# Kernel tuning notes

Hardware: AMD Instinct MI355X
Metric: run time of the kernel (lower is better)

## Reference

```python
import jax, jax.numpy as jnp
import numpy as np

N_NODES = 50000
N_EDGES = 600000
D_IN = 128
D_HID = 128
N_IDX = 4096


def gcn_conv(x, W, b, edge_index, num_nodes):
    """PyG GCNConv: add self loops, symmetric deg normalization, scatter-add, bias."""
    h = x @ W  # [N, D_out]
    loop = jnp.arange(num_nodes, dtype=edge_index.dtype)
    src = jnp.concatenate([edge_index[0], loop])
    dst = jnp.concatenate([edge_index[1], loop])
    deg = jax.ops.segment_sum(jnp.ones_like(dst, dtype=h.dtype), dst, num_segments=num_nodes)
    dinv = jnp.where(deg > 0, jax.lax.rsqrt(jnp.maximum(deg, 1.0)), 0.0)
    norm = dinv[src] * dinv[dst]  # [E+N]
    msgs = h[src] * norm[:, None]
    out = jax.ops.segment_sum(msgs, dst, num_segments=num_nodes)
    return out + b


def setup_inputs() -> dict:
    key = jax.random.key(0)
    ks = jax.random.split(key, 18)
    d = {
        "x": jax.random.normal(ks[0], (N_NODES, D_IN), dtype=jnp.float32),
        "syntactic_edge_index": jax.random.randint(ks[1], (2, N_EDGES), 0, N_NODES, dtype=jnp.int32),
        "sequential_edge_index": jax.random.randint(ks[2], (2, N_EDGES), 0, N_NODES, dtype=jnp.int32),
        "semantic_edge_index": jax.random.randint(ks[3], (2, N_EDGES), 0, N_NODES, dtype=jnp.int32),
        "index": jax.random.randint(ks[4], (N_IDX,), 0, N_NODES, dtype=jnp.int32),
    }
    s = 1.0 / np.sqrt(D_IN)
    names = ["syn", "seq", "sem"]
    for i, n in enumerate(names):
        d[f"w1_{n}"] = jax.random.uniform(ks[5 + i], (D_IN, D_HID), jnp.float32, -s, s)
        d[f"b1_{n}"] = jnp.zeros((D_HID,), jnp.float32)
        d[f"w2_{n}"] = jax.random.uniform(ks[8 + i], (D_HID, D_HID), jnp.float32, -s, s)
        d[f"b2_{n}"] = jnp.zeros((D_HID,), jnp.float32)
    return d


def reference(x, syntactic_edge_index, sequential_edge_index, semantic_edge_index, index,
              w1_syn, b1_syn, w1_seq, b1_seq, w1_sem, b1_sem,
              w2_syn, b2_syn, w2_seq, b2_seq, w2_sem, b2_sem):
    n = x.shape[0]
    # layer 1: three parallel GCN branches + ReLU (dropout is identity in eval mode)
    a = jax.nn.relu(gcn_conv(x, w1_syn, b1_syn, syntactic_edge_index, n))
    b = jax.nn.relu(gcn_conv(x, w1_seq, b1_seq, sequential_edge_index, n))
    c = jax.nn.relu(gcn_conv(x, w1_sem, b1_sem, semantic_edge_index, n))
    h = jnp.maximum(jnp.maximum(a, b), c)
    # layer 2
    a2 = jax.nn.relu(gcn_conv(h, w2_syn, b2_syn, syntactic_edge_index, n))
    b2 = jax.nn.relu(gcn_conv(h, w2_seq, b2_seq, sequential_edge_index, n))
    c2 = jax.nn.relu(gcn_conv(h, w2_sem, b2_sem, semantic_edge_index, n))
    out = jnp.maximum(jnp.maximum(a2, b2), c2)
    return out[index]
```

## Files before the change

### kernel.cpp

```cpp
#include <hip/hip_runtime.h>
#include <hip/hip_fp16.h>

#define NN 50000
#define NE 600000
#define NG 3
#define D  128
#define NI 4096
#define BW 1024
#define NBUCK 49
#define EPT_BIN 16
#define EPB_BIN (256 * EPT_BIN)
#define NBLK_BIN ((NE + EPB_BIN - 1) / EPB_BIN)

typedef _Float16 half8 __attribute__((ext_vector_type(8)));
typedef _Float16 half4v __attribute__((ext_vector_type(4)));
typedef float floatx4 __attribute__((ext_vector_type(4)));

static __device__ __forceinline__ float wextract(unsigned int v) {
  unsigned short u = (unsigned short)(v >> 16);
  _Float16 h;
  __builtin_memcpy(&h, &u, 2);
  return (float)h;
}

static __device__ __forceinline__ unsigned int packsw(int s, float w) {
  _Float16 h = (_Float16)w;
  unsigned short u;
  __builtin_memcpy(&u, &h, 2);
  return (unsigned int)s | ((unsigned int)u << 16);
}


__global__ __launch_bounds__(256) void xcvt_kernel(const float* __restrict__ x,
    __half* __restrict__ xh, int n2) {
  int i = blockIdx.x * 256 + threadIdx.x;
  if (i >= n2) return;
  float2 v = ((const float2*)x)[i];
  ((__half2*)xh)[i] = __floats2half2_rn(v.x, v.y);
}

__global__ __launch_bounds__(256) void wcvt_kernel(
    const float* __restrict__ W0, const float* __restrict__ W1, const float* __restrict__ W2,
    const float* __restrict__ W3, const float* __restrict__ W4, const float* __restrict__ W5,
    __half* __restrict__ Wf) {
  const float* Wm[6] = {W0, W1, W2, W3, W4, W5};
  int t = blockIdx.x * 256 + threadIdx.x;
  if (t >= 6 * 2048) return;
  int mat = t >> 11;
  int fr = (t >> 6) & 31;
  int lane = t & 63;
  int tt = fr >> 2, ks = fr & 3;
  int n = tt * 16 + (lane & 15);
  int kb = ks * 32 + (lane >> 4) * 8;
  const float* W = Wm[mat];
#pragma unroll
  for (int j = 0; j < 8; j++)
    Wf[(size_t)t * 8 + j] = __float2half(W[(kb + j) * 128 + n]);
}


__global__ __launch_bounds__(256) void count_kernel(const int* __restrict__ e0,
    const int* __restrict__ e1, const int* __restrict__ e2, int* __restrict__ bucketCnt) {
  __shared__ int cnt[NBUCK];
  int g = blockIdx.y;
  const int* ei = (g == 0) ? e0 : ((g == 1) ? e1 : e2);
  int tid = threadIdx.x;
  if (tid < NBUCK) cnt[tid] = 0;
  __syncthreads();
  int base = blockIdx.x * EPB_BIN;
#pragma unroll
  for (int i = 0; i < EPT_BIN; i++) {
    int e = base + tid + i * 256;
    if (e < NE) atomicAdd(&cnt[ei[NE + e] >> 10], 1);
  }
  __syncthreads();
  if (tid < NBUCK) atomicAdd(&bucketCnt[g * NBUCK + tid], cnt[tid]);
}

__global__ void bscan_kernel(const int* __restrict__ bucketCnt, int* __restrict__ bucketBase,
                             int* __restrict__ cursor, int* __restrict__ rp) {
  int g = threadIdx.x;
  if (g >= NG) return;
  int run = 0;
  for (int b = 0; b < NBUCK; b++) {
    int c = bucketCnt[g * NBUCK + b];
    bucketBase[g * NBUCK + b] = run;
    cursor[g * NBUCK + b] = run;
    run += c;
  }
  rp[g * (NN + 1) + NN] = NE;
}

__global__ __launch_bounds__(256) void bin_kernel(const int* __restrict__ e0,
    const int* __restrict__ e1, const int* __restrict__ e2,
    int* __restrict__ cursor, unsigned int* __restrict__ binned) {
  __shared__ int cnt[NBUCK];
  __shared__ int base[NBUCK];
  int g = blockIdx.y;
  const int* ei = (g == 0) ? e0 : ((g == 1) ? e1 : e2);
  int tid = threadIdx.x;
  if (tid < NBUCK) cnt[tid] = 0;
  __syncthreads();
  int estart = blockIdx.x * EPB_BIN;
  int src[EPT_BIN], dst[EPT_BIN], rk[EPT_BIN];
#pragma unroll
  for (int i = 0; i < EPT_BIN; i++) {
    int e = estart + tid + i * 256;
    if (e < NE) {
      src[i] = ei[e];
      dst[i] = ei[NE + e];
      rk[i] = atomicAdd(&cnt[dst[i] >> 10], 1);
    } else {
      rk[i] = -1;
    }
  }
  __syncthreads();
  if (tid < NBUCK) base[tid] = (cnt[tid] > 0) ? atomicAdd(&cursor[g * NBUCK + tid], cnt[tid]) : 0;
  __syncthreads();
#pragma unroll
  for (int i = 0; i < EPT_BIN; i++) {
    if (rk[i] >= 0) {
      int b = dst[i] >> 10;
      binned[(size_t)g * NE + base[b] + rk[i]] =
          (unsigned int)src[i] | ((unsigned int)dst[i] << 16);
    }
  }
}

__global__ __launch_bounds__(256) void csr_kernel(const unsigned int* __restrict__ binned,
    const int* __restrict__ bucketBase, const int* __restrict__ bucketCnt,
    int* __restrict__ rp, float* __restrict__ dinv) {
  __shared__ int deg[BW];
  __shared__ int wsum[4];
  int g = blockIdx.y, b = blockIdx.x;
  int tid = threadIdx.x;
  int node0 = b * BW;
  int bb = bucketBase[g * NBUCK + b];
  int total = bucketCnt[g * NBUCK + b];
  const unsigned int* bp = binned + (size_t)g * NE + bb;
  for (int i = tid; i < BW; i += 256) deg[i] = 0;
  __syncthreads();
  for (int e = tid; e < total; e += 256) {
    unsigned int p = bp[e];
    atomicAdd(&deg[(int)(p >> 16) - node0], 1);
  }
  __syncthreads();
  int d0 = deg[tid * 4], d1 = deg[tid * 4 + 1], d2 = deg[tid * 4 + 2], d3 = deg[tid * 4 + 3];
  int s = d0 + d1 + d2 + d3;
  int lane = tid & 63;
  int incl = s;
#pragma unroll
  for (int off = 1; off < 64; off <<= 1) {
    int n = __shfl_up(incl, off, 64);
    if (lane >= off) incl += n;
  }
  if (lane == 63) wsum[tid >> 6] = incl;
  __syncthreads();
  int wbase = 0;
#pragma unroll
  for (int w = 0; w < 4; w++)
    if (w < (tid >> 6)) wbase += wsum[w];
  int ex = wbase + incl - s;
  int exs[4] = {ex, ex + d0, ex + d0 + d1, ex + d0 + d1 + d2};
  int ds[4] = {d0, d1, d2, d3};
#pragma unroll
  for (int k = 0; k < 4; k++) {
    int node = node0 + tid * 4 + k;
    if (node < NN) {
      rp[g * (NN + 1) + node] = bb + exs[k];
      dinv[g * NN + node] = rsqrtf((float)ds[k] + 1.0f);
    }
  }
}

__global__ __launch_bounds__(256) void fillp_kernel(const unsigned int* __restrict__ binned,
    const int* __restrict__ bucketBase, const int* __restrict__ bucketCnt,
    const int* __restrict__ rp, const float* __restrict__ dinv,
    unsigned int* __restrict__ colp) {
  __shared__ int cur[BW];
  int g = blockIdx.y, b = blockIdx.x;
  int tid = threadIdx.x;
  int node0 = b * BW;
  int bb = bucketBase[g * NBUCK + b];
  int total = bucketCnt[g * NBUCK + b];
  const unsigned int* bp = binned + (size_t)g * NE + bb;
  for (int i = tid; i < BW; i += 256) {
    int node = node0 + i;
    cur[i] = (node < NN) ? rp[g * (NN + 1) + node] : 0;
  }
  __syncthreads();
  for (int e = tid; e < total; e += 256) {
    unsigned int p = bp[e];
    int srcid = (int)(p & 0xffffu);
    int r = atomicAdd(&cur[(int)(p >> 16) - node0], 1);
    colp[(size_t)g * NE + r] = packsw(srcid, dinv[g * NN + srcid]);
  }
}


__global__ __launch_bounds__(256) void aggf_kernel(
    const __half* __restrict__ srch, const int* __restrict__ rp,
    const unsigned int* __restrict__ colp, const float* __restrict__ dinv,
    const int* __restrict__ index, __half* __restrict__ tout, int nrows) {
  int w = (blockIdx.x * 256 + threadIdx.x) >> 6;
  if (w >= nrows) return;
  int lane = threadIdx.x & 63;
  int sub = lane >> 5;
  int fl = lane & 31;
  int node = index ? index[w] : w;
  const _Float16* srcv = (const _Float16*)srch;
  half4v selfh = *(const half4v*)&srcv[(size_t)node * D + fl * 4];
  float di0 = dinv[node], di1 = dinv[NN + node], di2 = dinv[2 * NN + node];
  float a0[4], a1[4], a2[4];
#pragma unroll
  for (int k = 0; k < 4; k++) {
    float sv = sub ? 0.f : (float)selfh[k];
    a0[k] = di0 * sv; a1[k] = di1 * sv; a2[k] = di2 * sv;
  }
  int s0 = rp[node],                e0 = rp[node + 1];
  int s1 = rp[(NN + 1) + node],     e1 = rp[(NN + 1) + node + 1];
  int s2 = rp[2 * (NN + 1) + node], e2 = rp[2 * (NN + 1) + node + 1];
  int n0 = e0 - s0, n1 = e1 - s1, n2 = e2 - s2;
  unsigned int c0 = (lane < n0) ? colp[s0 + lane] : 0u;
  unsigned int c1 = (lane < n1) ? colp[NE + s1 + lane] : 0u;
  unsigned int c2 = (lane < n2) ? colp[2 * NE + s2 + lane] : 0u;
  int m0 = min(n0, 64), m1 = min(n1, 64), m2 = min(n2, 64);
  int mx = max(m0, max(m1, m2));
  for (int j = 0; j < mx; j += 8) {
    half4v h0[4], h1[4], h2[4];
    float w0[4], w1[4], w2[4];
    bool p0 = j < m0, p1 = j < m1, p2 = j < m2;
    if (p0) {
#pragma unroll
      for (int u = 0; u < 4; u++) {
        unsigned int v = (unsigned int)__shfl((int)c0, j + u * 2 + sub, 64);
        w0[u] = wextract(v);
        h0[u] = *(const half4v*)&srcv[(size_t)(v & 0xffffu) * D + fl * 4];
      }
    }
    if (p1) {
#pragma unroll
      for (int u = 0; u < 4; u++) {
        unsigned int v = (unsigned int)__shfl((int)c1, j + u * 2 + sub, 64);
        w1[u] = wextract(v);
        h1[u] = *(const half4v*)&srcv[(size_t)(v & 0xffffu) * D + fl * 4];
      }
    }
    if (p2) {
#pragma unroll
      for (int u = 0; u < 4; u++) {
        unsigned int v = (unsigned int)__shfl((int)c2, j + u * 2 + sub, 64);
        w2[u] = wextract(v);
        h2[u] = *(const half4v*)&srcv[(size_t)(v & 0xffffu) * D + fl * 4];
      }
    }
    if (p0) {
#pragma unroll
      for (int u = 0; u < 4; u++)
#pragma unroll
        for (int k = 0; k < 4; k++) a0[k] = fmaf((float)h0[u][k], w0[u], a0[k]);
    }
    if (p1) {
#pragma unroll
      for (int u = 0; u < 4; u++)
#pragma unroll
        for (int k = 0; k < 4; k++) a1[k] = fmaf((float)h1[u][k], w1[u], a1[k]);
    }
    if (p2) {
#pragma unroll
      for (int u = 0; u < 4; u++)
#pragma unroll
        for (int k = 0; k < 4; k++) a2[k] = fmaf((float)h2[u][k], w2[u], a2[k]);
    }
  }
  for (int q = s0 + 64; q < e0; q += 64) {
    int nn = min(e0 - q, 64);
    unsigned int c = (lane < nn) ? colp[q + lane] : 0u;
    for (int j = 0; j < nn; j += 2) {
      unsigned int v = (unsigned int)__shfl((int)c, j + sub, 64);
      float wf = wextract(v);
      half4v hv = *(const half4v*)&srcv[(size_t)(v & 0xffffu) * D + fl * 4];
#pragma unroll
      for (int k = 0; k < 4; k++) a0[k] = fmaf((float)hv[k], wf, a0[k]);
    }
  }
  for (int q = s1 + 64; q < e1; q += 64) {
    int nn = min(e1 - q, 64);
    unsigned int c = (lane < nn) ? colp[NE + q + lane] : 0u;
    for (int j = 0; j < nn; j += 2) {
      unsigned int v = (unsigned int)__shfl((int)c, j + sub, 64);
      float wf = wextract(v);
      half4v hv = *(const half4v*)&srcv[(size_t)(v & 0xffffu) * D + fl * 4];
#pragma unroll
      for (int k = 0; k < 4; k++) a1[k] = fmaf((float)hv[k], wf, a1[k]);
    }
  }
  for (int q = s2 + 64; q < e2; q += 64) {
    int nn = min(e2 - q, 64);
    unsigned int c = (lane < nn) ? colp[2 * NE + q + lane] : 0u;
    for (int j = 0; j < nn; j += 2) {
      unsigned int v = (unsigned int)__shfl((int)c, j + sub, 64);
      float wf = wextract(v);
      half4v hv = *(const half4v*)&srcv[(size_t)(v & 0xffffu) * D + fl * 4];
#pragma unroll
      for (int k = 0; k < 4; k++) a2[k] = fmaf((float)hv[k], wf, a2[k]);
    }
  }
#pragma unroll
  for (int k = 0; k < 4; k++) {
    a0[k] += __shfl_xor(a0[k], 32, 64);
    a1[k] += __shfl_xor(a1[k], 32, 64);
    a2[k] += __shfl_xor(a2[k], 32, 64);
  }
  if (sub == 0) {
    size_t stride = (size_t)nrows * D;
    _Float16* tv = (_Float16*)tout;
    half4v o0, o1, o2;
#pragma unroll
    for (int k = 0; k < 4; k++) {
      o0[k] = (_Float16)(di0 * a0[k]);
      o1[k] = (_Float16)(di1 * a1[k]);
      o2[k] = (_Float16)(di2 * a2[k]);
    }
    *(half4v*)&tv[(size_t)w * D + fl * 4]              = o0;
    *(half4v*)&tv[stride + (size_t)w * D + fl * 4]     = o1;
    *(half4v*)&tv[2 * stride + (size_t)w * D + fl * 4] = o2;
  }
}


__global__ __launch_bounds__(256) void mmf_kernel(const __half* __restrict__ A,
    const __half* __restrict__ Wf,
    const float* __restrict__ B0, const float* __restrict__ B1, const float* __restrict__ B2,
    __half* __restrict__ outh, float* __restrict__ outf, int M) {
  __shared__ _Float16 Ws[16384];
  const float* Bb[3] = {B0, B1, B2};
  const int tid = threadIdx.x;
  const int wave = tid >> 6, lane = tid & 63;
  const int wr = (wave >> 1) * 64, wc = (wave & 1) * 64;
  const int ln = lane & 15, quad = lane >> 4;
  const int row_base = blockIdx.x * 128 + wr;
  float om[4][4][4];

  for (int b = 0; b < 3; b++) {
    const __half* Wb = Wf + (size_t)b * 16384;
#pragma unroll
    for (int i = 0; i < 8; i++) {
      int id = tid + i * 256;
      *(half8*)&Ws[id * 8] = *(const half8*)&Wb[(size_t)id * 8];
    }
    __syncthreads();

    const __half* Ab = A + (size_t)b * M * D;
    float bias[4];
#pragma unroll
    for (int ct = 0; ct < 4; ct++) bias[ct] = Bb[b][wc + ct * 16 + ln];
    floatx4 acc[4][4];
#pragma unroll
    for (int rt = 0; rt < 4; rt++)
#pragma unroll
      for (int ct = 0; ct < 4; ct++)
        acc[rt][ct] = (floatx4){bias[ct], bias[ct], bias[ct], bias[ct]};

#pragma unroll
    for (int ks = 0; ks < 4; ks++) {
      half8 av[4];
#pragma unroll
      for (int rt = 0; rt < 4; rt++) {
        int r = row_base + rt * 16 + ln;
        r = (r < M) ? r : (M - 1);
        av[rt] = *(const half8*)&Ab[(size_t)r * D + ks * 32 + quad * 8];
      }
#pragma unroll
      for (int ct = 0; ct < 4; ct++) {
        int tt = (wc >> 4) + ct;
        half8 bv = *(const half8*)&Ws[((tt * 4 + ks) * 64 + lane) * 8];
#pragma unroll
        for (int rt = 0; rt < 4; rt++)
          acc[rt][ct] = __builtin_amdgcn_mfma_f32_16x16x32_f16(av[rt], bv, acc[rt][ct], 0, 0, 0);
      }
    }
#pragma unroll
    for (int rt = 0; rt < 4; rt++)
#pragma unroll
      for (int ct = 0; ct < 4; ct++)
#pragma unroll
        for (int r = 0; r < 4; r++) {
          float v = fmaxf(acc[rt][ct][r], 0.f);
          om[rt][ct][r] = (b == 0) ? v : fmaxf(om[rt][ct][r], v);
        }
    __syncthreads();
  }
#pragma unroll
  for (int rt = 0; rt < 4; rt++) {
    int m = row_base + rt * 16 + quad * 4;
#pragma unroll
    for (int r = 0; r < 4; r++) {
      if (m + r < M) {
#pragma unroll
        for (int ct = 0; ct < 4; ct++) {
          int n = wc + ct * 16 + ln;
          if (outh) outh[(size_t)(m + r) * D + n] = __float2half(om[rt][ct][r]);
          else      outf[(size_t)(m + r) * D + n] = om[rt][ct][r];
        }
      }
    }
  }
}


extern "C" void kernel_launch(void* const* d_in, const int* in_sizes, int n_in,
                              void* d_out, int out_size, void* d_ws, size_t ws_size,
                              hipStream_t stream) {
  const float* x = (const float*)d_in[0];
  const int* e0 = (const int*)d_in[1];
  const int* e1 = (const int*)d_in[2];
  const int* e2 = (const int*)d_in[3];
  const int* index = (const int*)d_in[4];
  const float* w1[3] = {(const float*)d_in[5], (const float*)d_in[9],  (const float*)d_in[13]};
  const float* b1[3] = {(const float*)d_in[6], (const float*)d_in[10], (const float*)d_in[14]};
  const float* w2[3] = {(const float*)d_in[7], (const float*)d_in[11], (const float*)d_in[15]};
  const float* b2[3] = {(const float*)d_in[8], (const float*)d_in[12], (const float*)d_in[16]};
  float* out = (float*)d_out;

  char* ws = (char*)d_ws;
  size_t o = 0;
  auto alloc = [&](size_t bytes) {
    o = (o + 255) & ~(size_t)255;
    void* p = ws + o;
    o += bytes;
    return p;
  };
  int*    rp     = (int*)alloc((size_t)NG * (NN + 1) * 4);
  unsigned int* colp = (unsigned int*)alloc((size_t)NG * NE * 4);
  float*  dinv   = (float*)alloc((size_t)NG * NN * 4);
  int*    bcnt   = (int*)alloc((size_t)NG * NBUCK * 4);
  int*    bbase  = (int*)alloc((size_t)NG * NBUCK * 4);
  int*    bcur   = (int*)alloc((size_t)NG * NBUCK * 4);
  __half* xh     = (__half*)alloc((size_t)NN * D * 2);
  __half* Wf     = (__half*)alloc((size_t)6 * 128 * 128 * 2);
  __half* t1     = (__half*)alloc((size_t)NG * NN * D * 2);
  __half* hacc   = (__half*)alloc((size_t)NN * D * 2);
  unsigned int* binned = (unsigned int*)t1;
  __half* t2     = t1;
  (void)ws_size; (void)in_sizes; (void)n_in; (void)out_size;

  hipMemsetAsync(bcnt, 0, (size_t)NG * NBUCK * 4, stream);
  xcvt_kernel<<<(NN * D / 2 + 255) / 256, 256, 0, stream>>>(x, xh, NN * D / 2);
  wcvt_kernel<<<48, 256, 0, stream>>>(w1[0], w1[1], w1[2], w2[0], w2[1], w2[2], Wf);
  count_kernel<<<dim3(NBLK_BIN, NG), 256, 0, stream>>>(e0, e1, e2, bcnt);
  bscan_kernel<<<1, 64, 0, stream>>>(bcnt, bbase, bcur, rp);
  bin_kernel<<<dim3(NBLK_BIN, NG), 256, 0, stream>>>(e0, e1, e2, bcur, binned);
  csr_kernel<<<dim3(NBUCK, NG), 256, 0, stream>>>(binned, bbase, bcnt, rp, dinv);
  fillp_kernel<<<dim3(NBUCK, NG), 256, 0, stream>>>(binned, bbase, bcnt, rp, dinv, colp);

  aggf_kernel<<<(NN * 64 + 255) / 256, 256, 0, stream>>>(xh, rp, colp, dinv, nullptr, t1, NN);
  mmf_kernel<<<(NN + 127) / 128, 256, 0, stream>>>(t1, Wf, b1[0], b1[1], b1[2],
                                                   hacc, nullptr, NN);
  aggf_kernel<<<(NI * 64 + 255) / 256, 256, 0, stream>>>(hacc, rp, colp, dinv, index, t2, NI);
  mmf_kernel<<<(NI + 127) / 128, 256, 0, stream>>>(t2, Wf + (size_t)3 * 16384,
                                                   b2[0], b2[1], b2[2], nullptr, out, NI);
}
```

Baseline: 297.5 us.

## Fuse prep kernels, widen aggregation gathers to half8, stage A tile in LDS

Merges the x conversion, weight conversion and edge bucket counting into one prep kernel with block-range dispatch, removing two launches and vectorizing the x conversion to 8 elements per thread. The aggregation kernel now has each lane gather 8 halves (16 bytes), so four edges are processed at once per wave instead of two. This needs an extra cross-quarter shuffle reduction and more accumulator registers. The mmf kernel stages the 128x128 A tile into padded shared memory before the MFMA loop instead of reading it from global per wave, raising LDS use to about 67 KB, which may reduce occupancy.

```diff
diff --git a/kernel.cpp b/kernel.cpp
--- a/kernel.cpp
+++ b/kernel.cpp
@@ -11,9 +11,11 @@
 #define EPT_BIN 16
 #define EPB_BIN (256 * EPT_BIN)
 #define NBLK_BIN ((NE + EPB_BIN - 1) / EPB_BIN)
+#define XCVT_BLKS 3125
+#define WCVT_BLKS 48
+#define CNT_BLKS (NBLK_BIN * NG)
 
 typedef _Float16 half8 __attribute__((ext_vector_type(8)));
-typedef _Float16 half4v __attribute__((ext_vector_type(4)));
 typedef float floatx4 __attribute__((ext_vector_type(4)));
 
 static __device__ __forceinline__ float wextract(unsigned int v) {
@@ -31,50 +33,53 @@
 }
 
 
-__global__ __launch_bounds__(256) void xcvt_kernel(const float* __restrict__ x,
-    __half* __restrict__ xh, int n2) {
-  int i = blockIdx.x * 256 + threadIdx.x;
-  if (i >= n2) return;
-  float2 v = ((const float2*)x)[i];
-  ((__half2*)xh)[i] = __floats2half2_rn(v.x, v.y);
-}
-
-__global__ __launch_bounds__(256) void wcvt_kernel(
+__global__ __launch_bounds__(256) void prep_kernel(
+    const float* __restrict__ x, __half* __restrict__ xh,
     const float* __restrict__ W0, const float* __restrict__ W1, const float* __restrict__ W2,
     const float* __restrict__ W3, const float* __restrict__ W4, const float* __restrict__ W5,
-    __half* __restrict__ Wf) {
-  const float* Wm[6] = {W0, W1, W2, W3, W4, W5};
-  int t = blockIdx.x * 256 + threadIdx.x;
-  if (t >= 6 * 2048) return;
-  int mat = t >> 11;
-  int fr = (t >> 6) & 31;
-  int lane = t & 63;
-  int tt = fr >> 2, ks = fr & 3;
-  int n = tt * 16 + (lane & 15);
-  int kb = ks * 32 + (lane >> 4) * 8;
-  const float* W = Wm[mat];
-#pragma unroll
-  for (int j = 0; j < 8; j++)
-    Wf[(size_t)t * 8 + j] = __float2half(W[(kb + j) * 128 + n]);
-}
-
-
-__global__ __launch_bounds__(256) void count_kernel(const int* __restrict__ e0,
-    const int* __restrict__ e1, const int* __restrict__ e2, int* __restrict__ bucketCnt) {
+    __half* __restrict__ Wf,
+    const int* __restrict__ e0, const int* __restrict__ e1, const int* __restrict__ e2,
+    int* __restrict__ bucketCnt) {
   __shared__ int cnt[NBUCK];
-  int g = blockIdx.y;
-  const int* ei = (g == 0) ? e0 : ((g == 1) ? e1 : e2);
+  int blk = blockIdx.x;
   int tid = threadIdx.x;
-  if (tid < NBUCK) cnt[tid] = 0;
-  __syncthreads();
-  int base = blockIdx.x * EPB_BIN;
-#pragma unroll
-  for (int i = 0; i < EPT_BIN; i++) {
-    int e = base + tid + i * 256;
-    if (e < NE) atomicAdd(&cnt[ei[NE + e] >> 10], 1);
-  }
-  __syncthreads();
-  if (tid < NBUCK) atomicAdd(&bucketCnt[g * NBUCK + tid], cnt[tid]);
+  if (blk < XCVT_BLKS) {
+    int i = blk * 256 + tid;
+    size_t base = (size_t)i * 8;
+    float4 v0 = *(const float4*)&x[base];
+    float4 v1 = *(const float4*)&x[base + 4];
+    half8 h;
+    h[0] = (_Float16)v0.x; h[1] = (_Float16)v0.y; h[2] = (_Float16)v0.z; h[3] = (_Float16)v0.w;
+    h[4] = (_Float16)v1.x; h[5] = (_Float16)v1.y; h[6] = (_Float16)v1.z; h[7] = (_Float16)v1.w;
+    *(half8*)&xh[base] = h;
+  } else if (blk < XCVT_BLKS + WCVT_BLKS) {
+    const float* Wm[6] = {W0, W1, W2, W3, W4, W5};
+    int t = (blk - XCVT_BLKS) * 256 + tid;
+    int mat = t >> 11;
+    int fr = (t >> 6) & 31;
+    int lane = t & 63;
+    int tt = fr >> 2, ks = fr & 3;
+    int n = tt * 16 + (lane & 15);
+    int kb = ks * 32 + (lane >> 4) * 8;
+    const float* W = Wm[mat];
+#pragma unroll
+    for (int j = 0; j < 8; j++)
+      Wf[(size_t)t * 8 + j] = __float2half(W[(kb + j) * 128 + n]);
+  } else {
+    int cb = blk - XCVT_BLKS - WCVT_BLKS;
+    int g = cb / NBLK_BIN, eb = cb % NBLK_BIN;
+    const int* ei = (g == 0) ? e0 : ((g == 1) ? e1 : e2);
+    if (tid < NBUCK) cnt[tid] = 0;
+    __syncthreads();
+    int base = eb * EPB_BIN;
+#pragma unroll
+    for (int i = 0; i < EPT_BIN; i++) {
+      int e = base + tid + i * 256;
+      if (e < NE) atomicAdd(&cnt[ei[NE + e] >> 10], 1);
+    }
+    __syncthreads();
+    if (tid < NBUCK) atomicAdd(&bucketCnt[g * NBUCK + tid], cnt[tid]);
+  }
 }
 
 __global__ void bscan_kernel(const int* __restrict__ bucketCnt, int* __restrict__ bucketBase,
@@ -205,16 +210,16 @@
   int w = (blockIdx.x * 256 + threadIdx.x) >> 6;
   if (w >= nrows) return;
   int lane = threadIdx.x & 63;
-  int sub = lane >> 5;
-  int fl = lane & 31;
+  int q = lane >> 4;
+  int fl = lane & 15;
   int node = index ? index[w] : w;
   const _Float16* srcv = (const _Float16*)srch;
-  half4v selfh = *(const half4v*)&srcv[(size_t)node * D + fl * 4];
   float di0 = dinv[node], di1 = dinv[NN + node], di2 = dinv[2 * NN + node];
-  float a0[4], a1[4], a2[4];
-#pragma unroll
-  for (int k = 0; k < 4; k++) {
-    float sv = sub ? 0.f : (float)selfh[k];
+  half8 selfh = *(const half8*)&srcv[(size_t)node * D + fl * 8];
+  float a0[8], a1[8], a2[8];
+#pragma unroll
+  for (int k = 0; k < 8; k++) {
+    float sv = (q == 0) ? (float)selfh[k] : 0.f;
     a0[k] = di0 * sv; a1[k] = di1 * sv; a2[k] = di2 * sv;
   }
   int s0 = rp[node],                e0 = rp[node + 1];
@@ -226,120 +231,127 @@
   unsigned int c2 = (lane < n2) ? colp[2 * NE + s2 + lane] : 0u;
   int m0 = min(n0, 64), m1 = min(n1, 64), m2 = min(n2, 64);
   int mx = max(m0, max(m1, m2));
-  for (int j = 0; j < mx; j += 8) {
-    half4v h0[4], h1[4], h2[4];
+  for (int j = 0; j < mx; j += 16) {
+    bool p0 = j < m0, p1 = j < m1, p2 = j < m2;
+    unsigned int v0[4], v1[4], v2[4];
+    half8 h0[4], h1[4], h2[4];
     float w0[4], w1[4], w2[4];
-    bool p0 = j < m0, p1 = j < m1, p2 = j < m2;
     if (p0) {
 #pragma unroll
       for (int u = 0; u < 4; u++) {
-        unsigned int v = (unsigned int)__shfl((int)c0, j + u * 2 + sub, 64);
-        w0[u] = wextract(v);
-        h0[u] = *(const half4v*)&srcv[(size_t)(v & 0xffffu) * D + fl * 4];
+        v0[u] = (unsigned int)__shfl((int)c0, j + u * 4 + q, 64);
+        w0[u] = wextract(v0[u]);
+        h0[u] = *(const half8*)&srcv[(size_t)(v0[u] & 0xffffu) * D + fl * 8];
       }
     }
     if (p1) {
 #pragma unroll
       for (int u = 0; u < 4; u++) {
-        unsigned int v = (unsigned int)__shfl((int)c1, j + u * 2 + sub, 64);
-        w1[u] = wextract(v);
-        h1[u] = *(const half4v*)&srcv[(size_t)(v & 0xffffu) * D + fl * 4];
+        v1[u] = (unsigned int)__shfl((int)c1, j + u * 4 + q, 64);
+        w1[u] = wextract(v1[u]);
+        h1[u] = *(const half8*)&srcv[(size_t)(v1[u] & 0xffffu) * D + fl * 8];
       }
     }
     if (p2) {
 #pragma unroll
       for (int u = 0; u < 4; u++) {
-        unsigned int v = (unsigned int)__shfl((int)c2, j + u * 2 + sub, 64);
-        w2[u] = wextract(v);
-        h2[u] = *(const half4v*)&srcv[(size_t)(v & 0xffffu) * D + fl * 4];
+        v2[u] = (unsigned int)__shfl((int)c2, j + u * 4 + q, 64);
+        w2[u] = wextract(v2[u]);
+        h2[u] = *(const half8*)&srcv[(size_t)(v2[u] & 0xffffu) * D + fl * 8];
       }
     }
     if (p0) {
 #pragma unroll
       for (int u = 0; u < 4; u++)
 #pragma unroll
-        for (int k = 0; k < 4; k++) a0[k] = fmaf((float)h0[u][k], w0[u], a0[k]);
+        for (int k = 0; k < 8; k++) a0[k] = fmaf((float)h0[u][k], w0[u], a0[k]);
     }
     if (p1) {
 #pragma unroll
       for (int u = 0; u < 4; u++)
 #pragma unroll
-        for (int k = 0; k < 4; k++) a1[k] = fmaf((float)h1[u][k], w1[u], a1[k]);
+        for (int k = 0; k < 8; k++) a1[k] = fmaf((float)h1[u][k], w1[u], a1[k]);
     }
     if (p2) {
 #pragma unroll
       for (int u = 0; u < 4; u++)
 #pragma unroll
-        for (int k = 0; k < 4; k++) a2[k] = fmaf((float)h2[u][k], w2[u], a2[k]);
-    }
-  }
-  for (int q = s0 + 64; q < e0; q += 64) {
-    int nn = min(e0 - q, 64);
-    unsigned int c = (lane < nn) ? colp[q + lane] : 0u;
-    for (int j = 0; j < nn; j += 2) {
-      unsigned int v = (unsigned int)__shfl((int)c, j + sub, 64);
+        for (int k = 0; k < 8; k++) a2[k] = fmaf((float)h2[u][k], w2[u], a2[k]);
+    }
+  }
+  for (int p = s0 + 64; p < e0; p += 64) {
+    int nn = min(e0 - p, 64);
+    unsigned int c = (lane < nn) ? colp[p + lane] : 0u;
+    for (int j = 0; j < nn; j += 4) {
+      unsigned int v = (unsigned int)__shfl((int)c, j + q, 64);
       float wf = wextract(v);
-      half4v hv = *(const half4v*)&srcv[(size_t)(v & 0xffffu) * D + fl * 4];
-#pragma unroll
-      for (int k = 0; k < 4; k++) a0[k] = fmaf((float)hv[k], wf, a0[k]);
-    }
-  }
-  for (int q = s1 + 64; q < e1; q += 64) {
-    int nn = min(e1 - q, 64);
-    unsigned int c = (lane < nn) ? colp[NE + q + lane] : 0u;
-    for (int j = 0; j < nn; j += 2) {
-      unsigned int v = (unsigned int)__shfl((int)c, j + sub, 64);
+      half8 hv = *(const half8*)&srcv[(size_t)(v & 0xffffu) * D + fl * 8];
+#pragma unroll
+      for (int k = 0; k < 8; k++) a0[k] = fmaf((float)hv[k], wf, a0[k]);
+    }
+  }
+  for (int p = s1 + 64; p < e1; p += 64) {
+    int nn = min(e1 - p, 64);
+    unsigned int c = (lane < nn) ? colp[NE + p + lane] : 0u;
+    for (int j = 0; j < nn; j += 4) {
+      unsigned int v = (unsigned int)__shfl((int)c, j + q, 64);
       float wf = wextract(v);
-      half4v hv = *(const half4v*)&srcv[(size_t)(v & 0xffffu) * D + fl * 4];
-#pragma unroll
-      for (int k = 0; k < 4; k++) a1[k] = fmaf((float)hv[k], wf, a1[k]);
-    }
-  }
-  for (int q = s2 + 64; q < e2; q += 64) {
-    int nn = min(e2 - q, 64);
-    unsigned int c = (lane < nn) ? colp[2 * NE + q + lane] : 0u;
-    for (int j = 0; j < nn; j += 2) {
-      unsigned int v = (unsigned int)__shfl((int)c, j + sub, 64);
+      half8 hv = *(const half8*)&srcv[(size_t)(v & 0xffffu) * D + fl * 8];
+#pragma unroll
+      for (int k = 0; k < 8; k++) a1[k] = fmaf((float)hv[k], wf, a1[k]);
+    }
+  }
+  for (int p = s2 + 64; p < e2; p += 64) {
+    int nn = min(e2 - p, 64);
+    unsigned int c = (lane < nn) ? colp[2 * NE + p + lane] : 0u;
+    for (int j = 0; j < nn; j += 4) {
+      unsigned int v = (unsigned int)__shfl((int)c, j + q, 64);
       float wf = wextract(v);
-      half4v hv = *(const half4v*)&srcv[(size_t)(v & 0xffffu) * D + fl * 4];
-#pragma unroll
-      for (int k = 0; k < 4; k++) a2[k] = fmaf((float)hv[k], wf, a2[k]);
-    }
-  }
-#pragma unroll
-  for (int k = 0; k < 4; k++) {
+      half8 hv = *(const half8*)&srcv[(size_t)(v & 0xffffu) * D + fl * 8];
+#pragma unroll
+      for (int k = 0; k < 8; k++) a2[k] = fmaf((float)hv[k], wf, a2[k]);
+    }
+  }
+#pragma unroll
+  for (int k = 0; k < 8; k++) {
+    a0[k] += __shfl_xor(a0[k], 16, 64);
     a0[k] += __shfl_xor(a0[k], 32, 64);
+    a1[k] += __shfl_xor(a1[k], 16, 64);
     a1[k] += __shfl_xor(a1[k], 32, 64);
+    a2[k] += __shfl_xor(a2[k], 16, 64);
     a2[k] += __shfl_xor(a2[k], 32, 64);
   }
-  if (sub == 0) {
+  if (q == 0) {
     size_t stride = (size_t)nrows * D;
     _Float16* tv = (_Float16*)tout;
-    half4v o0, o1, o2;
-#pragma unroll
-    for (int k = 0; k < 4; k++) {
+    half8 o0, o1, o2;
+#pragma unroll
+    for (int k = 0; k < 8; k++) {
       o0[k] = (_Float16)(di0 * a0[k]);
       o1[k] = (_Float16)(di1 * a1[k]);
       o2[k] = (_Float16)(di2 * a2[k]);
     }
-    *(half4v*)&tv[(size_t)w * D + fl * 4]              = o0;
-    *(half4v*)&tv[stride + (size_t)w * D + fl * 4]     = o1;
-    *(half4v*)&tv[2 * stride + (size_t)w * D + fl * 4] = o2;
-  }
-}
-
+    *(half8*)&tv[(size_t)w * D + fl * 8]              = o0;
+    *(half8*)&tv[stride + (size_t)w * D + fl * 8]     = o1;
+    *(half8*)&tv[2 * stride + (size_t)w * D + fl * 8] = o2;
+  }
+}
+
+
+#define ALD 136
 
 __global__ __launch_bounds__(256) void mmf_kernel(const __half* __restrict__ A,
     const __half* __restrict__ Wf,
     const float* __restrict__ B0, const float* __restrict__ B1, const float* __restrict__ B2,
     __half* __restrict__ outh, float* __restrict__ outf, int M) {
+  __shared__ _Float16 As[128 * ALD];
   __shared__ _Float16 Ws[16384];
   const float* Bb[3] = {B0, B1, B2};
   const int tid = threadIdx.x;
   const int wave = tid >> 6, lane = tid & 63;
   const int wr = (wave >> 1) * 64, wc = (wave & 1) * 64;
   const int ln = lane & 15, quad = lane >> 4;
-  const int row_base = blockIdx.x * 128 + wr;
+  const int row0 = blockIdx.x * 128;
   float om[4][4][4];
 
   for (int b = 0; b < 3; b++) {
@@ -349,9 +361,18 @@
       int id = tid + i * 256;
       *(half8*)&Ws[id * 8] = *(const half8*)&Wb[(size_t)id * 8];
     }
+    const __half* Ab = A + (size_t)b * M * D;
+#pragma unroll
+    for (int i = 0; i < 8; i++) {
+      int idx = tid + i * 256;
+      int r = idx >> 4, c8 = idx & 15;
+      int gr = row0 + r;
+      gr = (gr < M) ? gr : (M - 1);
+      half8 v = *(const half8*)&Ab[(size_t)gr * D + c8 * 8];
+      *(half8*)&As[r * ALD + c8 * 8] = v;
+    }
     __syncthreads();
 
-    const __half* Ab = A + (size_t)b * M * D;
     float bias[4];
 #pragma unroll
     for (int ct = 0; ct < 4; ct++) bias[ct] = Bb[b][wc + ct * 16 + ln];
@@ -366,11 +387,8 @@
     for (int ks = 0; ks < 4; ks++) {
       half8 av[4];
 #pragma unroll
-      for (int rt = 0; rt < 4; rt++) {
-        int r = row_base + rt * 16 + ln;
-        r = (r < M) ? r : (M - 1);
-        av[rt] = *(const half8*)&Ab[(size_t)r * D + ks * 32 + quad * 8];
-      }
+      for (int rt = 0; rt < 4; rt++)
+        av[rt] = *(const half8*)&As[(wr + rt * 16 + ln) * ALD + ks * 32 + quad * 8];
 #pragma unroll
       for (int ct = 0; ct < 4; ct++) {
         int tt = (wc >> 4) + ct;
@@ -393,7 +411,7 @@
   }
 #pragma unroll
   for (int rt = 0; rt < 4; rt++) {
-    int m = row_base + rt * 16 + quad * 4;
+    int m = row0 + wr + rt * 16 + quad * 4;
 #pragma unroll
     for (int r = 0; r < 4; r++) {
       if (m + r < M) {
@@ -446,9 +464,8 @@
   (void)ws_size; (void)in_sizes; (void)n_in; (void)out_size;
 
   hipMemsetAsync(bcnt, 0, (size_t)NG * NBUCK * 4, stream);
-  xcvt_kernel<<<(NN * D / 2 + 255) / 256, 256, 0, stream>>>(x, xh, NN * D / 2);
-  wcvt_kernel<<<48, 256, 0, stream>>>(w1[0], w1[1], w1[2], w2[0], w2[1], w2[2], Wf);
-  count_kernel<<<dim3(NBLK_BIN, NG), 256, 0, stream>>>(e0, e1, e2, bcnt);
+  prep_kernel<<<XCVT_BLKS + WCVT_BLKS + CNT_BLKS, 256, 0, stream>>>(
+      x, xh, w1[0], w1[1], w1[2], w2[0], w2[1], w2[2], Wf, e0, e1, e2, bcnt);
   bscan_kernel<<<1, 64, 0, stream>>>(bcnt, bbase, bcur, rp);
   bin_kernel<<<dim3(NBLK_BIN, NG), 256, 0, stream>>>(e0, e1, e2, bcur, binned);
   csr_kernel<<<dim3(NBUCK, NG), 256, 0, stream>>>(binned, bbase, bcnt, rp, dinv);
```

After: 301.4 us. Within noise of the previous version (+1.3%).

## Fuse prep kernels, use per-wave bin counters, stage A tiles in LDS

Applied to the files above, without the earlier changes.

Merges the x conversion, weight conversion and edge counting into one launch, and widens the x conversion to 8 elements per thread. The binning kernel now keeps separate shared counters for each wave, which reduces atomic contention on the shared counters. The matmul kernel stages each 128-row A tile into padded LDS with coalesced loads instead of strided global loads per MFMA fragment. This raises LDS usage per block (about 66KB), which may lower occupancy.

```diff
diff --git a/kernel.cpp b/kernel.cpp
--- a/kernel.cpp
+++ b/kernel.cpp
@@ -11,6 +11,9 @@
 #define EPT_BIN 16
 #define EPB_BIN (256 * EPT_BIN)
 #define NBLK_BIN ((NE + EPB_BIN - 1) / EPB_BIN)
+#define XCVT_BLKS 3125
+#define WCVT_BLKS 48
+#define CNT_BLKS (NBLK_BIN * NG)
 
 typedef _Float16 half8 __attribute__((ext_vector_type(8)));
 typedef _Float16 half4v __attribute__((ext_vector_type(4)));
@@ -31,50 +34,53 @@
 }
 
 
-__global__ __launch_bounds__(256) void xcvt_kernel(const float* __restrict__ x,
-    __half* __restrict__ xh, int n2) {
-  int i = blockIdx.x * 256 + threadIdx.x;
-  if (i >= n2) return;
-  float2 v = ((const float2*)x)[i];
-  ((__half2*)xh)[i] = __floats2half2_rn(v.x, v.y);
-}
-
-__global__ __launch_bounds__(256) void wcvt_kernel(
+__global__ __launch_bounds__(256) void prep_kernel(
+    const float* __restrict__ x, __half* __restrict__ xh,
     const float* __restrict__ W0, const float* __restrict__ W1, const float* __restrict__ W2,
     const float* __restrict__ W3, const float* __restrict__ W4, const float* __restrict__ W5,
-    __half* __restrict__ Wf) {
-  const float* Wm[6] = {W0, W1, W2, W3, W4, W5};
-  int t = blockIdx.x * 256 + threadIdx.x;
-  if (t >= 6 * 2048) return;
-  int mat = t >> 11;
-  int fr = (t >> 6) & 31;
-  int lane = t & 63;
-  int tt = fr >> 2, ks = fr & 3;
-  int n = tt * 16 + (lane & 15);
-  int kb = ks * 32 + (lane >> 4) * 8;
-  const float* W = Wm[mat];
-#pragma unroll
-  for (int j = 0; j < 8; j++)
-    Wf[(size_t)t * 8 + j] = __float2half(W[(kb + j) * 128 + n]);
-}
-
-
-__global__ __launch_bounds__(256) void count_kernel(const int* __restrict__ e0,
-    const int* __restrict__ e1, const int* __restrict__ e2, int* __restrict__ bucketCnt) {
+    __half* __restrict__ Wf,
+    const int* __restrict__ e0, const int* __restrict__ e1, const int* __restrict__ e2,
+    int* __restrict__ bucketCnt) {
   __shared__ int cnt[NBUCK];
-  int g = blockIdx.y;
-  const int* ei = (g == 0) ? e0 : ((g == 1) ? e1 : e2);
+  int blk = blockIdx.x;
   int tid = threadIdx.x;
-  if (tid < NBUCK) cnt[tid] = 0;
-  __syncthreads();
-  int base = blockIdx.x * EPB_BIN;
-#pragma unroll
-  for (int i = 0; i < EPT_BIN; i++) {
-    int e = base + tid + i * 256;
-    if (e < NE) atomicAdd(&cnt[ei[NE + e] >> 10], 1);
-  }
-  __syncthreads();
-  if (tid < NBUCK) atomicAdd(&bucketCnt[g * NBUCK + tid], cnt[tid]);
+  if (blk < XCVT_BLKS) {
+    int i = blk * 256 + tid;
+    size_t base = (size_t)i * 8;
+    float4 v0 = *(const float4*)&x[base];
+    float4 v1 = *(const float4*)&x[base + 4];
+    half8 h;
+    h[0] = (_Float16)v0.x; h[1] = (_Float16)v0.y; h[2] = (_Float16)v0.z; h[3] = (_Float16)v0.w;
+    h[4] = (_Float16)v1.x; h[5] = (_Float16)v1.y; h[6] = (_Float16)v1.z; h[7] = (_Float16)v1.w;
+    *(half8*)&xh[base] = h;
+  } else if (blk < XCVT_BLKS + WCVT_BLKS) {
+    const float* Wm[6] = {W0, W1, W2, W3, W4, W5};
+    int t = (blk - XCVT_BLKS) * 256 + tid;
+    int mat = t >> 11;
+    int fr = (t >> 6) & 31;
+    int lane = t & 63;
+    int tt = fr >> 2, ks = fr & 3;
+    int n = tt * 16 + (lane & 15);
+    int kb = ks * 32 + (lane >> 4) * 8;
+    const float* W = Wm[mat];
+#pragma unroll
+    for (int j = 0; j < 8; j++)
+      Wf[(size_t)t * 8 + j] = __float2half(W[(kb + j) * 128 + n]);
+  } else {
+    int cb = blk - XCVT_BLKS - WCVT_BLKS;
+    int g = cb / NBLK_BIN, eb = cb % NBLK_BIN;
+    const int* ei = (g == 0) ? e0 : ((g == 1) ? e1 : e2);
+    if (tid < NBUCK) cnt[tid] = 0;
+    __syncthreads();
+    int base = eb * EPB_BIN;
+#pragma unroll
+    for (int i = 0; i < EPT_BIN; i++) {
+      int e = base + tid + i * 256;
+      if (e < NE) atomicAdd(&cnt[ei[NE + e] >> 10], 1);
+    }
+    __syncthreads();
+    if (tid < NBUCK) atomicAdd(&bucketCnt[g * NBUCK + tid], cnt[tid]);
+  }
 }
 
 __global__ void bscan_kernel(const int* __restrict__ bucketCnt, int* __restrict__ bucketBase,
@@ -94,12 +100,14 @@
 __global__ __launch_bounds__(256) void bin_kernel(const int* __restrict__ e0,
     const int* __restrict__ e1, const int* __restrict__ e2,
     int* __restrict__ cursor, unsigned int* __restrict__ binned) {
-  __shared__ int cnt[NBUCK];
+  __shared__ int cnt[4][NBUCK];
   __shared__ int base[NBUCK];
+  __shared__ int woff[4][NBUCK];
   int g = blockIdx.y;
   const int* ei = (g == 0) ? e0 : ((g == 1) ? e1 : e2);
   int tid = threadIdx.x;
-  if (tid < NBUCK) cnt[tid] = 0;
+  int wave = tid >> 6;
+  if (tid < NBUCK) { cnt[0][tid] = 0; cnt[1][tid] = 0; cnt[2][tid] = 0; cnt[3][tid] = 0; }
   __syncthreads();
   int estart = blockIdx.x * EPB_BIN;
   int src[EPT_BIN], dst[EPT_BIN], rk[EPT_BIN];
@@ -109,19 +117,24 @@
     if (e < NE) {
       src[i] = ei[e];
       dst[i] = ei[NE + e];
-      rk[i] = atomicAdd(&cnt[dst[i] >> 10], 1);
+      rk[i] = atomicAdd(&cnt[wave][dst[i] >> 10], 1);
     } else {
       rk[i] = -1;
     }
   }
   __syncthreads();
-  if (tid < NBUCK) base[tid] = (cnt[tid] > 0) ? atomicAdd(&cursor[g * NBUCK + tid], cnt[tid]) : 0;
+  if (tid < NBUCK) {
+    int c0 = cnt[0][tid], c1 = cnt[1][tid], c2 = cnt[2][tid], c3 = cnt[3][tid];
+    int total = c0 + c1 + c2 + c3;
+    base[tid] = (total > 0) ? atomicAdd(&cursor[g * NBUCK + tid], total) : 0;
+    woff[0][tid] = 0; woff[1][tid] = c0; woff[2][tid] = c0 + c1; woff[3][tid] = c0 + c1 + c2;
+  }
   __syncthreads();
 #pragma unroll
   for (int i = 0; i < EPT_BIN; i++) {
     if (rk[i] >= 0) {
       int b = dst[i] >> 10;
-      binned[(size_t)g * NE + base[b] + rk[i]] =
+      binned[(size_t)g * NE + base[b] + woff[wave][b] + rk[i]] =
           (unsigned int)src[i] | ((unsigned int)dst[i] << 16);
     }
   }
@@ -329,17 +342,20 @@
 }
 
 
+#define ALD 136
+
 __global__ __launch_bounds__(256) void mmf_kernel(const __half* __restrict__ A,
     const __half* __restrict__ Wf,
     const float* __restrict__ B0, const float* __restrict__ B1, const float* __restrict__ B2,
     __half* __restrict__ outh, float* __restrict__ outf, int M) {
+  __shared__ _Float16 As[128 * ALD];
   __shared__ _Float16 Ws[16384];
   const float* Bb[3] = {B0, B1, B2};
   const int tid = threadIdx.x;
   const int wave = tid >> 6, lane = tid & 63;
   const int wr = (wave >> 1) * 64, wc = (wave & 1) * 64;
   const int ln = lane & 15, quad = lane >> 4;
-  const int row_base = blockIdx.x * 128 + wr;
+  const int row0 = blockIdx.x * 128;
   float om[4][4][4];
 
   for (int b = 0; b < 3; b++) {
@@ -349,9 +365,18 @@
       int id = tid + i * 256;
       *(half8*)&Ws[id * 8] = *(const half8*)&Wb[(size_t)id * 8];
     }
+    const __half* Ab = A + (size_t)b * M * D;
+#pragma unroll
+    for (int i = 0; i < 8; i++) {
+      int idx = tid + i * 256;
+      int r = idx >> 4, c8 = idx & 15;
+      int gr = row0 + r;
+      gr = (gr < M) ? gr : (M - 1);
+      half8 v = *(const half8*)&Ab[(size_t)gr * D + c8 * 8];
+      *(half8*)&As[r * ALD + c8 * 8] = v;
+    }
     __syncthreads();
 
-    const __half* Ab = A + (size_t)b * M * D;
     float bias[4];
 #pragma unroll
     for (int ct = 0; ct < 4; ct++) bias[ct] = Bb[b][wc + ct * 16 + ln];
@@ -366,11 +391,8 @@
     for (int ks = 0; ks < 4; ks++) {
       half8 av[4];
 #pragma unroll
-      for (int rt = 0; rt < 4; rt++) {
-        int r = row_base + rt * 16 + ln;
-        r = (r < M) ? r : (M - 1);
-        av[rt] = *(const half8*)&Ab[(size_t)r * D + ks * 32 + quad * 8];
-      }
+      for (int rt = 0; rt < 4; rt++)
+        av[rt] = *(const half8*)&As[(wr + rt * 16 + ln) * ALD + ks * 32 + quad * 8];
 #pragma unroll
       for (int ct = 0; ct < 4; ct++) {
         int tt = (wc >> 4) + ct;
@@ -393,7 +415,7 @@
   }
 #pragma unroll
   for (int rt = 0; rt < 4; rt++) {
-    int m = row_base + rt * 16 + quad * 4;
+    int m = row0 + wr + rt * 16 + quad * 4;
 #pragma unroll
     for (int r = 0; r < 4; r++) {
       if (m + r < M) {
@@ -446,9 +468,8 @@
   (void)ws_size; (void)in_sizes; (void)n_in; (void)out_size;
 
   hipMemsetAsync(bcnt, 0, (size_t)NG * NBUCK * 4, stream);
-  xcvt_kernel<<<(NN * D / 2 + 255) / 256, 256, 0, stream>>>(x, xh, NN * D / 2);
-  wcvt_kernel<<<48, 256, 0, stream>>>(w1[0], w1[1], w1[2], w2[0], w2[1], w2[2], Wf);
-  count_kernel<<<dim3(NBLK_BIN, NG), 256, 0, stream>>>(e0, e1, e2, bcnt);
+  prep_kernel<<<XCVT_BLKS + WCVT_BLKS + CNT_BLKS, 256, 0, stream>>>(
+      x, xh, w1[0], w1[1], w1[2], w2[0], w2[1], w2[2], Wf, e0, e1, e2, bcnt);
   bscan_kernel<<<1, 64, 0, stream>>>(bcnt, bbase, bcur, rp);
   bin_kernel<<<dim3(NBLK_BIN, NG), 256, 0, stream>>>(e0, e1, e2, bcur, binned);
   csr_kernel<<<dim3(NBUCK, NG), 256, 0, stream>>>(binned, bbase, bcnt, rp, dinv);
```

Result: faster. 283.7 us (-4.6%).
